# Kernel optimization log

Hardware: AMD Instinct MI355X
Metric: run time of the kernel (lower is better)

## Reference

```python
import jax, jax.numpy as jnp
import numpy as np

N, D, E = 200000, 256, 6400000
RATIO = 0.5
NEG_SLOPE = 0.2


def _xavier(key, shape, gain=1.414):
    fan_in, fan_out = shape[0], shape[1]
    limit = gain * (6.0 / (fan_in + fan_out)) ** 0.5
    return jax.random.uniform(key, shape, jnp.float32, -limit, limit)


def setup_inputs() -> dict:
    key = jax.random.key(0)
    ks = jax.random.split(key, 8)
    x = jax.random.normal(ks[0], (N, D), jnp.float32)
    edge_index = jax.random.randint(ks[1], (2, E), 0, N, dtype=jnp.int64)
    return {
        "x": x,
        "edge_index": edge_index,
        "w_s1": _xavier(ks[2], (2 * D, D)), "b_s1": jnp.zeros((D,), jnp.float32),
        "w_s2": _xavier(ks[3], (D, 1)),     "b_s2": jnp.zeros((1,), jnp.float32),
        "w_f1": _xavier(ks[4], (D, D // 2)), "b_f1": jnp.zeros((D // 2,), jnp.float32),
        "w_f2": _xavier(ks[5], (D // 2, 1)), "b_f2": jnp.zeros((1,), jnp.float32),
        "w_p": _xavier(ks[6], (D, D)),      "b_p": jnp.zeros((D,), jnp.float32),
        "alpha": jnp.float32(0.5), "beta": jnp.float32(0.5),
    }


def reference(x, edge_index, w_s1, b_s1, w_s2, b_s2, w_f1, b_f1, w_f2, b_f2, w_p, b_p, alpha, beta):
    num_nodes = x.shape[0]
    k = max(1, int(RATIO * num_nodes))
    lrelu = lambda v: jax.nn.leaky_relu(v, NEG_SLOPE)

    row, col = edge_index[0], edge_index[1]
    # degree(row, N): scatter-add of ones over source nodes
    deg = jax.ops.segment_sum(jnp.ones_like(row, dtype=x.dtype), row, num_segments=num_nodes)
    # F.normalize(p=2, dim=0) on the [N,1] degree column
    deg_norm = deg / jnp.maximum(jnp.sqrt(jnp.sum(deg * deg)), 1e-12)

    struct_in = jnp.concatenate([x, jnp.broadcast_to(deg_norm[:, None], x.shape)], axis=1)  # [N, 2D]
    struct_scores = (lrelu(struct_in @ w_s1 + b_s1) @ w_s2 + b_s2)[:, 0]  # dropout is eval no-op
    feat_scores = (lrelu(x @ w_f1 + b_f1) @ w_f2 + b_f2)[:, 0]

    a = jax.nn.sigmoid(alpha)
    b = jax.nn.sigmoid(beta)
    s = a + b
    scores = (a / s) * struct_scores + (b / s) * feat_scores  # [N]

    # single-graph top-k (batch=None default path)
    topk_scores, topk_idx = jax.lax.top_k(scores, k)
    x_pooled = lrelu(x[topk_idx] @ w_p + b_p)  # post_pool, dropout no-op

    # edge remap + compaction (valid edges first, -1 padding to keep static shape)
    node_map = jnp.full((num_nodes,), -1, dtype=jnp.int32).at[topk_idx].set(
        jnp.arange(k, dtype=jnp.int32))
    mr, mc = node_map[row], node_map[col]
    mask = (mr >= 0) & (mc >= 0)
    order = jnp.argsort(~mask, stable=True)  # stable: keeps original edge order among valid
    edge_index_pooled = jnp.stack([
        jnp.where(mask, mr, -1)[order],
        jnp.where(mask, mc, -1)[order],
    ])
    return x_pooled, edge_index_pooled, topk_scores
```

## Files before the change

kernel.cpp:

```cpp
#include <hip/hip_runtime.h>
#include <math.h>

typedef unsigned long long u64;
typedef unsigned int u32;
typedef unsigned short u16;
typedef __attribute__((ext_vector_type(8))) short bf16x8;
typedef __attribute__((ext_vector_type(4))) float f32x4;

#define D   256
#define ECH 16
#define EBLK (256*ECH)
#define BAND_W 4096
#define BAND_DELTA 1e-3f
#define HR  25088
#define HCH 32

__device__ __forceinline__ double lrelu(double v){ return v > 0.0 ? v : 0.2*v; }
__device__ __forceinline__ float  lreluf(float v){ return v > 0.0f ? v : 0.2f*v; }

__device__ __forceinline__ u16 f2bf(float f){
  union{float f; u32 u;} v; v.f = f;
  u32 r = v.u + 0x7FFFu + ((v.u >> 16) & 1u);
  return (u16)(r >> 16);
}
__device__ __forceinline__ float bf2f(u16 b){
  union{u32 u; float f;} v; v.u = ((u32)b) << 16; return v.f;
}

__global__ __launch_bounds__(256) void k_deghist(const int* __restrict__ row, int E,
                                                 u32* __restrict__ partial, int NR){
  __shared__ u32 h[HR/2];
  const int tid = threadIdx.x;
  const int r = blockIdx.x % NR;
  const int c = blockIdx.x / NR;
  for (int i = tid; i < HR/2; i += 256) h[i] = 0;
  __syncthreads();
  const int lo = r * HR;
  int CE = ((E + HCH - 1) / HCH + 3) & ~3;
  const int e0 = c * CE;
  const int e1 = min(e0 + CE, E);
  for (int e = e0 + tid*4; e < e1; e += 256*4){
    if (e + 3 < e1){
      int4 v = *(const int4*)(row + e);
      u32 d0 = (u32)(v.x - lo), d1 = (u32)(v.y - lo);
      u32 d2 = (u32)(v.z - lo), d3 = (u32)(v.w - lo);
      if (d0 < (u32)HR) atomicAdd(&h[d0 >> 1], 1u << ((d0 & 1)*16));
      if (d1 < (u32)HR) atomicAdd(&h[d1 >> 1], 1u << ((d1 & 1)*16));
      if (d2 < (u32)HR) atomicAdd(&h[d2 >> 1], 1u << ((d2 & 1)*16));
      if (d3 < (u32)HR) atomicAdd(&h[d3 >> 1], 1u << ((d3 & 1)*16));
    } else {
      for (int j = 0; j < 4 && e + j < e1; ++j){
        u32 d = (u32)(row[e+j] - lo);
        if (d < (u32)HR) atomicAdd(&h[d >> 1], 1u << ((d & 1)*16));
      }
    }
  }
  __syncthreads();
  u32* plane = partial + (size_t)blockIdx.x * (HR/2);
  for (int i = tid; i < HR/2; i += 256) plane[i] = h[i];
}

__global__ void k_degred2(const u32* __restrict__ partial, int N, int NR,
                          int* __restrict__ deg, u64* __restrict__ out){
  __shared__ u64 sh[256];
  u64 local = 0;
  int stride = gridDim.x*blockDim.x;
  for (int i = blockIdx.x*blockDim.x + threadIdx.x; i < N; i += stride){
    int r = i / HR, off = i % HR;
    const int word = off >> 1, shift = (off & 1)*16;
    u32 s = 0;
    #pragma unroll 8
    for (int c = 0; c < HCH; ++c)
      s += (partial[(size_t)(c*NR + r)*(HR/2) + word] >> shift) & 0xFFFFu;
    deg[i] = (int)s;
    local += (u64)s * (u64)s;
  }
  sh[threadIdx.x] = local; __syncthreads();
  for (int s = 128; s > 0; s >>= 1){
    if (threadIdx.x < s) sh[threadIdx.x] += sh[threadIdx.x+s];
    __syncthreads();
  }
  if (threadIdx.x == 0) atomicAdd(out, sh[0]);
}

__global__ void k_prep_wsw(const float* __restrict__ wS1, const float* __restrict__ wF1,
                           const float* __restrict__ wP,
                           const float* __restrict__ alpha, const float* __restrict__ beta,
                           const u64* __restrict__ sumsq,
                           u16* __restrict__ wswH, u16* __restrict__ wswL,
                           u16* __restrict__ wPH,
                           double* __restrict__ s1b, double* __restrict__ scal,
                           float* __restrict__ s1bf, float* __restrict__ scalf){
  const int b = blockIdx.x;
  if (b < 384){
    int idx = b*256 + threadIdx.x;
    int i    = idx & 7;
    int lane = (idx >> 3) & 63;
    int sg   = (idx >> 9) & 7;
    int t    = idx >> 12;
    int k = sg*32 + ((lane >> 4) & 3)*8 + i;
    int c16 = lane & 15;
    float wv;
    if (t < 16) wv = wS1[k*256 + t*16 + c16];
    else        wv = wF1[k*128 + (t-16)*16 + c16];
    u16 h = f2bf(wv);
    wswH[idx] = h;
    wswL[idx] = f2bf(wv - bf2f(h));
  } else if (b < 640){
    int idx = (b-384)*256 + threadIdx.x;
    int i    = idx & 7;
    int lane = (idx >> 3) & 63;
    int sg   = (idx >> 9) & 7;
    int t    = idx >> 12;
    int k = sg*32 + ((lane >> 4) & 3)*8 + i;
    wPH[idx] = f2bf(wP[k*256 + t*16 + (lane & 15)]);
  } else {
    int j = threadIdx.x;
    double s = 0.0;
    for (int r = 0; r < D; ++r) s += (double)wS1[(D + r)*D + j];
    s1b[j] = s;
    s1bf[j] = (float)s;
    if (j == 0){
      double a = 1.0/(1.0 + exp(-(double)alpha[0]));
      double bb = 1.0/(1.0 + exp(-(double)beta[0]));
      scal[0] = a/(a+bb);
      scal[1] = bb/(a+bb);
      double dn = sqrt((double)(*sumsq));
      scal[2] = dn > 1e-12 ? dn : 1e-12;
      scalf[0] = (float)scal[0];
      scalf[1] = (float)scal[1];
      scalf[2] = (float)(1.0/scal[2]);
    }
  }
}

__global__ __launch_bounds__(512, 4) void k_scores_mfma(
    const float* __restrict__ x, const int* __restrict__ deg,
    const u16* __restrict__ wswH, const u16* __restrict__ wswL,
    const float* __restrict__ bS1, const float* __restrict__ wS2, const float* __restrict__ bS2,
    const float* __restrict__ bF1, const float* __restrict__ wF2, const float* __restrict__ bF2,
    const float* __restrict__ s1bf, const float* __restrict__ scalf,
    float* __restrict__ s32, u64* __restrict__ keys, int N, int SORTN)
{
  __shared__ u16 xsh[2][4096];
  __shared__ u16 xsl[2][4096];
  __shared__ float dnsh[64];
  __shared__ float part_s[64][9];
  __shared__ float part_f[64][9];

  const int tid  = threadIdx.x;
  const int lane = tid & 63;
  const int w    = tid >> 6;
  const int node0 = blockIdx.x * 64;

  if (node0 >= N){
    if (tid < 64){
      int i = node0 + tid;
      if (i < SORTN) keys[i] = ~0ULL;
    }
    return;
  }

  if (tid < 64){
    int node = node0 + tid;
    dnsh[tid] = (node < N) ? ((float)deg[node] * scalf[2]) : 0.0f;
  }

  const int row_st = tid >> 3;
  const int seg_st = tid & 7;
  const int unit_w = row_st*8 + (seg_st ^ (row_st & 7));
  const float* srcbase = x + (size_t)(node0 + row_st)*D + seg_st*8;
  const bool rv = (node0 + row_st) < N;

  f32x4 acc[4][3];
  #pragma unroll
  for (int m = 0; m < 4; ++m)
    #pragma unroll
    for (int n = 0; n < 3; ++n) acc[m][n] = (f32x4){0.f,0.f,0.f,0.f};

  float xr[8];
  {
    if (rv){
      float4 a = *(const float4*)(srcbase);
      float4 b = *(const float4*)(srcbase + 4);
      xr[0]=a.x; xr[1]=a.y; xr[2]=a.z; xr[3]=a.w;
      xr[4]=b.x; xr[5]=b.y; xr[6]=b.z; xr[7]=b.w;
    } else {
      #pragma unroll
      for (int i = 0; i < 8; ++i) xr[i] = 0.f;
    }
  }

  #pragma unroll
  for (int c = 0; c < 4; ++c){
    const int pb = c & 1;
    {
      u16 h[8];
      #pragma unroll
      for (int i = 0; i < 8; ++i) h[i] = f2bf(xr[i]);
      uint4 H; H.x = (u32)h[0] | ((u32)h[1]<<16); H.y = (u32)h[2] | ((u32)h[3]<<16);
               H.z = (u32)h[4] | ((u32)h[5]<<16); H.w = (u32)h[6] | ((u32)h[7]<<16);
      u16 l[8];
      #pragma unroll
      for (int i = 0; i < 8; ++i) l[i] = f2bf(xr[i] - bf2f(h[i]));
      uint4 L; L.x = (u32)l[0] | ((u32)l[1]<<16); L.y = (u32)l[2] | ((u32)l[3]<<16);
               L.z = (u32)l[4] | ((u32)l[5]<<16); L.w = (u32)l[6] | ((u32)l[7]<<16);
      *(uint4*)&xsh[pb][unit_w*8] = H;
      *(uint4*)&xsl[pb][unit_w*8] = L;
    }
    __syncthreads();
    if (c < 3){
      const float* sn = srcbase + (c+1)*64;
      if (rv){
        float4 a = *(const float4*)(sn);
        float4 b = *(const float4*)(sn + 4);
        xr[0]=a.x; xr[1]=a.y; xr[2]=a.z; xr[3]=a.w;
        xr[4]=b.x; xr[5]=b.y; xr[6]=b.z; xr[7]=b.w;
      }
    }
    #pragma unroll
    for (int s = 0; s < 2; ++s){
      const int sg = c*2 + s;
      bf16x8 ah[4], al[4];
      #pragma unroll
      for (int mt = 0; mt < 4; ++mt){
        int row = mt*16 + (lane & 15);
        int seg = s*4 + (lane >> 4);
        int un  = row*8 + (seg ^ (row & 7));
        ah[mt] = *(const bf16x8*)&xsh[pb][un*8];
        al[mt] = *(const bf16x8*)&xsl[pb][un*8];
      }
      const int t0 = w*3;
      size_t o0 = ((size_t)(t0*8 + sg)*64 + lane)*8;
      bf16x8 bh = *(const bf16x8*)&wswH[o0];
      bf16x8 bl = *(const bf16x8*)&wswL[o0];
      #pragma unroll
      for (int nt = 0; nt < 3; ++nt){
        bf16x8 nbh = bh, nbl = bl;
        if (nt < 2){
          size_t on = ((size_t)((t0+nt+1)*8 + sg)*64 + lane)*8;
          nbh = *(const bf16x8*)&wswH[on];
          nbl = *(const bf16x8*)&wswL[on];
        }
        #pragma unroll
        for (int mt = 0; mt < 4; ++mt){
          acc[mt][nt] = __builtin_amdgcn_mfma_f32_16x16x32_bf16(ah[mt], bh, acc[mt][nt], 0,0,0);
          acc[mt][nt] = __builtin_amdgcn_mfma_f32_16x16x32_bf16(al[mt], bh, acc[mt][nt], 0,0,0);
          acc[mt][nt] = __builtin_amdgcn_mfma_f32_16x16x32_bf16(ah[mt], bl, acc[mt][nt], 0,0,0);
        }
        bh = nbh; bl = nbl;
      }
    }
    if (c < 3) __syncthreads();
  }

  float dnl[4][4];
  #pragma unroll
  for (int mt = 0; mt < 4; ++mt)
    #pragma unroll
    for (int j = 0; j < 4; ++j)
      dnl[mt][j] = dnsh[mt*16 + (lane>>4)*4 + j];

  float ps[4][4], pf[4][4];
  #pragma unroll
  for (int mt = 0; mt < 4; ++mt)
    #pragma unroll
    for (int j = 0; j < 4; ++j){ ps[mt][j] = 0.f; pf[mt][j] = 0.f; }

  #pragma unroll
  for (int nt = 0; nt < 3; ++nt){
    const int t = w*3 + nt;
    const int c16 = lane & 15;
    const bool isS = (t < 16);
    const int col = isS ? t*16 + c16 : (t-16)*16 + c16;
    const float bias = isS ? bS1[col] : bF1[col];
    const float sbv  = isS ? s1bf[col] : 0.f;
    const float vv   = isS ? wS2[col] : wF2[col];
    #pragma unroll
    for (int mt = 0; mt < 4; ++mt){
      #pragma unroll
      for (int j = 0; j < 4; ++j){
        float v = acc[mt][nt][j] + bias + dnl[mt][j]*sbv;
        v = lreluf(v) * vv;
        v += __shfl_xor(v, 1);
        v += __shfl_xor(v, 2);
        v += __shfl_xor(v, 4);
        v += __shfl_xor(v, 8);
        if (isS) ps[mt][j] += v; else pf[mt][j] += v;
      }
    }
  }
  if ((lane & 15) == 0){
    #pragma unroll
    for (int mt = 0; mt < 4; ++mt)
      #pragma unroll
      for (int j = 0; j < 4; ++j){
        int row = mt*16 + (lane>>4)*4 + j;
        part_s[row][w] = ps[mt][j];
        part_f[row][w] = pf[mt][j];
      }
  }
  __syncthreads();
  if (tid < 64){
    int node = node0 + tid;
    if (node < N){
      float sv = 0.f, fv = 0.f;
      #pragma unroll
      for (int ww = 0; ww < 8; ++ww){ sv += part_s[tid][ww]; fv += part_f[tid][ww]; }
      float sc = scalf[0]*(sv + bS2[0]) + scalf[1]*(fv + bF2[0]);
      s32[node] = sc;
      u32 bits = __float_as_uint(sc);
      u32 ord = (bits >> 31) ? ~bits : (bits | 0x80000000u);
      keys[node] = ((u64)(~ord) << 32) | (u32)node;
    } else {
      int i = node0 + tid;
      if (i < SORTN) keys[i] = ~0ULL;
    }
  }
}

__global__ __launch_bounds__(1024) void k_bsort_local8k(u64* __restrict__ keys){
  __shared__ u64 sk[8192];
  const int tid = threadIdx.x;
  const int base = blockIdx.x * 8192;
  #pragma unroll
  for (int e = 0; e < 8; ++e) sk[tid + e*1024] = keys[base + tid + e*1024];
  __syncthreads();
  for (int size = 2; size <= 8192; size <<= 1){
    for (int stride = size >> 1; stride > 0; stride >>= 1){
      #pragma unroll
      for (int pp = 0; pp < 4; ++pp){
        int p  = tid + pp*1024;
        int i  = 2*p - (p & (stride-1));
        int jj = i + stride;
        bool up = (((base + i) & size) == 0);
        u64 ki = sk[i], kj = sk[jj];
        if ((ki > kj) == up){ sk[i] = kj; sk[jj] = ki; }
      }
      __syncthreads();
    }
  }
  #pragma unroll
  for (int e = 0; e < 8; ++e) keys[base + tid + e*1024] = sk[tid + e*1024];
}

__global__ __launch_bounds__(1024) void k_bmerge_local8k(u64* __restrict__ keys, int size){
  __shared__ u64 sk[8192];
  const int tid = threadIdx.x;
  const int base = blockIdx.x * 8192;
  #pragma unroll
  for (int e = 0; e < 8; ++e) sk[tid + e*1024] = keys[base + tid + e*1024];
  __syncthreads();
  for (int stride = 4096; stride > 0; stride >>= 1){
    #pragma unroll
    for (int pp = 0; pp < 4; ++pp){
      int p  = tid + pp*1024;
      int i  = 2*p - (p & (stride-1));
      int jj = i + stride;
      bool up = (((base + i) & size) == 0);
      u64 ki = sk[i], kj = sk[jj];
      if ((ki > kj) == up){ sk[i] = kj; sk[jj] = ki; }
    }
    __syncthreads();
  }
  #pragma unroll
  for (int e = 0; e < 8; ++e) keys[base + tid + e*1024] = sk[tid + e*1024];
}

template<int NS>
__global__ void k_bpassM(u64* __restrict__ keys, int size, int stride){
  const int G = 1 << NS;
  u32 t = blockIdx.x*blockDim.x + threadIdx.x;
  u32 smin = (u32)stride >> (NS-1);
  u32 i0 = (t/smin)*(smin << NS) + (t % smin);
  u64 v[G];
  #pragma unroll
  for (int j = 0; j < G; ++j) v[j] = keys[i0 + (u32)j*smin];
  bool up = ((i0 & (u32)size) == 0);
  #pragma unroll
  for (int b = (G>>1); b >= 1; b >>= 1){
    #pragma unroll
    for (int j = 0; j < G; ++j){
      if ((j & b) == 0){
        u64 a = v[j], cc = v[j|b];
        if ((a > cc) == up){ v[j] = cc; v[j|b] = a; }
      }
    }
  }
  #pragma unroll
  for (int j = 0; j < G; ++j) keys[i0 + (u32)j*smin] = v[j];
}

__global__ void kr_cut(const u64* __restrict__ keys, int k, float* __restrict__ cutbuf,
                       int* __restrict__ r01){
  if (threadIdx.x == 0 && blockIdx.x == 0){
    u32 key32 = (u32)(keys[k-1] >> 32);
    u32 ord = ~key32;
    u32 u = (ord & 0x80000000u) ? (ord ^ 0x80000000u) : ~ord;
    float c = __uint_as_float(u);
    cutbuf[0] = c - BAND_DELTA;
    cutbuf[1] = c + BAND_DELTA;
    r01[0] = 0x7FFFFFFF;
    r01[1] = -1;
  }
}

__global__ __launch_bounds__(256) void kr_rescore(
    const u64* __restrict__ keys, const float* __restrict__ s32,
    const float* __restrict__ x, const int* __restrict__ deg,
    const float* __restrict__ wS1, const float* __restrict__ bS1,
    const float* __restrict__ wS2, const float* __restrict__ bS2,
    const float* __restrict__ wF1, const float* __restrict__ bF1,
    const float* __restrict__ wF2, const float* __restrict__ bF2,
    const double* __restrict__ s1b, const double* __restrict__ scal,
    const float* __restrict__ cutbuf, int* __restrict__ r01,
    double* __restrict__ bandS, int k, int N)
{
  const int r = k - BAND_W + blockIdx.x;
  if (r < 0 || r >= N) return;
  const int node = (int)(u32)(keys[r] & 0xFFFFFFFFULL);
  const float s = s32[node];
  if (s < cutbuf[0] || s > cutbuf[1]) return;

  const int tid = threadIdx.x;
  if (tid == 0){ atomicMin(&r01[0], r); atomicMax(&r01[1], r); }

  __shared__ float xr[256];
  __shared__ double rsp[4], rfp[4];
  xr[tid] = x[(size_t)node*D + tid];
  __syncthreads();

  const int j = tid;
  double a0=0.0, a1=0.0, a2=0.0, a3=0.0;
  double b0=0.0, b1=0.0, b2=0.0, b3=0.0;
  if (j < 128){
    for (int rr = 0; rr < D; rr += 4){
      double x0 = (double)xr[rr+0], x1 = (double)xr[rr+1];
      double x2 = (double)xr[rr+2], x3 = (double)xr[rr+3];
      a0 = fma(x0, (double)wS1[(rr+0)*D + j], a0);
      a1 = fma(x1, (double)wS1[(rr+1)*D + j], a1);
      a2 = fma(x2, (double)wS1[(rr+2)*D + j], a2);
      a3 = fma(x3, (double)wS1[(rr+3)*D + j], a3);
      b0 = fma(x0, (double)wF1[(rr+0)*128 + j], b0);
      b1 = fma(x1, (double)wF1[(rr+1)*128 + j], b1);
      b2 = fma(x2, (double)wF1[(rr+2)*128 + j], b2);
      b3 = fma(x3, (double)wF1[(rr+3)*128 + j], b3);
    }
  } else {
    for (int rr = 0; rr < D; rr += 4){
      double x0 = (double)xr[rr+0], x1 = (double)xr[rr+1];
      double x2 = (double)xr[rr+2], x3 = (double)xr[rr+3];
      a0 = fma(x0, (double)wS1[(rr+0)*D + j], a0);
      a1 = fma(x1, (double)wS1[(rr+1)*D + j], a1);
      a2 = fma(x2, (double)wS1[(rr+2)*D + j], a2);
      a3 = fma(x3, (double)wS1[(rr+3)*D + j], a3);
    }
  }
  double accA = ((a0+a1)+(a2+a3)) + (double)bS1[j] + ((double)deg[node]/scal[2]) * s1b[j];
  double sp = lrelu(accA) * (double)wS2[j];
  double fp = 0.0;
  if (j < 128){
    double accB = ((b0+b1)+(b2+b3)) + (double)bF1[j];
    fp = lrelu(accB) * (double)wF2[j];
  }

  const int lane = tid & 63, wave = tid >> 6;
  #pragma unroll
  for (int off = 32; off > 0; off >>= 1){
    sp += __shfl_down(sp, off);
    fp += __shfl_down(fp, off);
  }
  if (lane == 0){ rsp[wave] = sp; rfp[wave] = fp; }
  __syncthreads();
  if (tid == 0){
    double SP = rsp[0]+rsp[1]+rsp[2]+rsp[3];
    double FP = rfp[0]+rfp[1]+rfp[2]+rfp[3];
    bandS[blockIdx.x] = scal[0]*(SP + (double)bS2[0]) + scal[1]*(FP + (double)bF2[0]);
  }
}

__global__ __launch_bounds__(1024) void kr_bandsort(u64* __restrict__ keys,
    const double* __restrict__ bandS, const int* __restrict__ r01, int k){
  __shared__ double bs[8192];
  __shared__ int bi[8192];
  const int r0 = r01[0], r1 = r01[1];
  int nb = r1 - r0 + 1;
  if (nb <= 1) return;
  if (nb > 8192) nb = 8192;
  int M = 1; while (M < nb) M <<= 1;
  const int tid = threadIdx.x;
  const int sbase = r0 - (k - BAND_W);
  for (int m = tid; m < M; m += 1024){
    if (m < nb){ bs[m] = bandS[sbase + m]; bi[m] = (int)(u32)(keys[r0+m] & 0xFFFFFFFFULL); }
    else       { bs[m] = -1.0/0.0;         bi[m] = 0x7FFFFFFF; }
  }
  __syncthreads();
  for (int size = 2; size <= M; size <<= 1){
    for (int stride = size >> 1; stride > 0; stride >>= 1){
      for (int p = tid; p < (M >> 1); p += 1024){
        int i = 2*p - (p & (stride-1));
        int jj = i + stride;
        bool up = ((i & size) == 0);
        double si_ = bs[i], sj = bs[jj];
        int ii = bi[i], ij = bi[jj];
        bool gt = (si_ < sj) || (si_ == sj && ii > ij);
        if (gt == up){ bs[i]=sj; bs[jj]=si_; bi[i]=ij; bi[jj]=ii; }
      }
      __syncthreads();
    }
  }
  for (int m = tid; m < nb; m += 1024)
    keys[r0+m] = (u64)(u32)bi[m];
}

__global__ void k_finalize(const u64* __restrict__ keys, const float* __restrict__ s32,
                           int k, int* __restrict__ nmap, float* __restrict__ outS){
  int p = blockIdx.x*blockDim.x + threadIdx.x;
  if (p < k){
    int node = (int)(u32)(keys[p] & 0xFFFFFFFFULL);
    nmap[node] = p;
    outS[p] = s32[node];
  }
}

__global__ __launch_bounds__(512, 4) void k_xpool_mfma(
    const float* __restrict__ x, const u64* __restrict__ keys,
    const u16* __restrict__ wH,
    const float* __restrict__ bP, float* __restrict__ out, int kk)
{
  __shared__ u16 xsh[2][4096];

  const int tid  = threadIdx.x;
  const int lane = tid & 63;
  const int w    = tid >> 6;
  const int p0 = blockIdx.x * 64;
  if (p0 >= kk) return;

  const int row_st = tid >> 3;
  const int seg_st = tid & 7;
  const int unit_w = row_st*8 + (seg_st ^ (row_st & 7));
  int prow = p0 + row_st; if (prow >= kk) prow = kk - 1;
  const int node = (int)(u32)(keys[prow] & 0xFFFFFFFFULL);
  const float* srcbase = x + (size_t)node*D + seg_st*8;

  f32x4 acc[4][2];
  #pragma unroll
  for (int m = 0; m < 4; ++m){ acc[m][0] = (f32x4){0.f,0.f,0.f,0.f}; acc[m][1] = (f32x4){0.f,0.f,0.f,0.f}; }

  float xr[8];
  {
    float4 a = *(const float4*)(srcbase);
    float4 b = *(const float4*)(srcbase + 4);
    xr[0]=a.x; xr[1]=a.y; xr[2]=a.z; xr[3]=a.w;
    xr[4]=b.x; xr[5]=b.y; xr[6]=b.z; xr[7]=b.w;
  }

  #pragma unroll
  for (int c = 0; c < 4; ++c){
    const int pb = c & 1;
    {
      u16 h[8];
      #pragma unroll
      for (int i = 0; i < 8; ++i) h[i] = f2bf(xr[i]);
      uint4 H; H.x = (u32)h[0] | ((u32)h[1]<<16); H.y = (u32)h[2] | ((u32)h[3]<<16);
               H.z = (u32)h[4] | ((u32)h[5]<<16); H.w = (u32)h[6] | ((u32)h[7]<<16);
      *(uint4*)&xsh[pb][unit_w*8] = H;
    }
    __syncthreads();
    if (c < 3){
      const float* sn = srcbase + (c+1)*64;
      float4 a = *(const float4*)(sn);
      float4 b = *(const float4*)(sn + 4);
      xr[0]=a.x; xr[1]=a.y; xr[2]=a.z; xr[3]=a.w;
      xr[4]=b.x; xr[5]=b.y; xr[6]=b.z; xr[7]=b.w;
    }
    #pragma unroll
    for (int s = 0; s < 2; ++s){
      const int sg = c*2 + s;
      bf16x8 ah[4];
      #pragma unroll
      for (int mt = 0; mt < 4; ++mt){
        int row = mt*16 + (lane & 15);
        int seg = s*4 + (lane >> 4);
        int un  = row*8 + (seg ^ (row & 7));
        ah[mt] = *(const bf16x8*)&xsh[pb][un*8];
      }
      const int t0 = w*2;
      size_t o0 = ((size_t)(t0*8 + sg)*64 + lane)*8;
      bf16x8 bh = *(const bf16x8*)&wH[o0];
      #pragma unroll
      for (int nt = 0; nt < 2; ++nt){
        bf16x8 nbh = bh;
        if (nt < 1){
          size_t on = ((size_t)((t0+1)*8 + sg)*64 + lane)*8;
          nbh = *(const bf16x8*)&wH[on];
        }
        #pragma unroll
        for (int mt = 0; mt < 4; ++mt)
          acc[mt][nt] = __builtin_amdgcn_mfma_f32_16x16x32_bf16(ah[mt], bh, acc[mt][nt], 0,0,0);
        bh = nbh;
      }
    }
    if (c < 3) __syncthreads();
  }

  const int c16 = lane & 15, r4 = (lane >> 4)*4;
  #pragma unroll
  for (int nt = 0; nt < 2; ++nt){
    const int col = (w*2 + nt)*16 + c16;
    const float bias = bP[col];
    #pragma unroll
    for (int mt = 0; mt < 4; ++mt){
      #pragma unroll
      for (int j = 0; j < 4; ++j){
        int p = p0 + mt*16 + r4 + j;
        if (p < kk) out[(size_t)p*D + col] = lreluf(acc[mt][nt][j] + bias);
      }
    }
  }
}

__global__ __launch_bounds__(256) void k_ecount(const int* __restrict__ erow, const int* __restrict__ ecol,
    const int* __restrict__ nmap, int E, int* __restrict__ bcount){
  __shared__ int sc[256];
  const int tid = threadIdx.x;
  const int base = blockIdx.x*EBLK + tid*ECH;
  int cnt = 0;
  #pragma unroll
  for (int q = 0; q < ECH; ++q){
    int e = base + q;
    if (e < E){
      if (nmap[erow[e]] >= 0 && nmap[ecol[e]] >= 0) cnt++;
    }
  }
  sc[tid] = cnt; __syncthreads();
  for (int s = 128; s > 0; s >>= 1){
    if (tid < s) sc[tid] += sc[tid+s];
    __syncthreads();
  }
  if (tid == 0) bcount[blockIdx.x] = sc[0];
}

__global__ __launch_bounds__(1024) void k_escan(const int* __restrict__ bcount, int nblk,
                                                int* __restrict__ boff, int* __restrict__ tot){
  __shared__ int sh[1024];
  const int tid = threadIdx.x;
  int carry = 0;
  for (int s = 0; s < nblk; s += 1024){
    int v = (s + tid < nblk) ? bcount[s+tid] : 0;
    sh[tid] = v; __syncthreads();
    for (int d = 1; d < 1024; d <<= 1){
      int t = (tid >= d) ? sh[tid-d] : 0;
      __syncthreads();
      sh[tid] += t;
      __syncthreads();
    }
    if (s + tid < nblk) boff[s+tid] = carry + sh[tid] - v;
    carry += sh[1023];
    __syncthreads();
  }
  if (tid == 0) *tot = carry;
}

__global__ void k_efill_tail(float* __restrict__ outR, float* __restrict__ outC,
                             const int* __restrict__ tot, int E){
  const int t0 = *tot;
  int stride = gridDim.x*blockDim.x;
  for (int i = t0 + blockIdx.x*blockDim.x + threadIdx.x; i < E; i += stride){
    outR[i] = -1.0f;
    outC[i] = -1.0f;
  }
}

__global__ __launch_bounds__(256) void k_escatter(const int* __restrict__ erow, const int* __restrict__ ecol,
    const int* __restrict__ nmap, int E, const int* __restrict__ boff,
    float* __restrict__ outR, float* __restrict__ outC){
  __shared__ int sc[256];
  const int tid = threadIdx.x;
  const int base = blockIdx.x*EBLK + tid*ECH;
  int mr[ECH], mc[ECH];
  int cnt = 0;
  #pragma unroll
  for (int q = 0; q < ECH; ++q){
    int e = base + q;
    int a = -1, b = -1;
    if (e < E){ a = nmap[erow[e]]; b = nmap[ecol[e]]; }
    mr[q] = a; mc[q] = b;
    if (a >= 0 && b >= 0) cnt++;
  }
  sc[tid] = cnt; __syncthreads();
  int v = cnt;
  for (int d = 1; d < 256; d <<= 1){
    int t = (tid >= d) ? sc[tid-d] : 0;
    __syncthreads();
    sc[tid] += t;
    __syncthreads();
  }
  int pos = boff[blockIdx.x] + sc[tid] - v;
  #pragma unroll
  for (int q = 0; q < ECH; ++q){
    if (mr[q] >= 0 && mc[q] >= 0){
      outR[pos] = (float)mr[q];
      outC[pos] = (float)mc[q];
      pos++;
    }
  }
}

extern "C" void kernel_launch(void* const* d_in, const int* in_sizes, int n_in,
                              void* d_out, int out_size, void* d_ws, size_t ws_size,
                              hipStream_t stream)
{
  const float* x   = (const float*)d_in[0];
  const int*   ei  = (const int*)d_in[1];
  const float* wS1 = (const float*)d_in[2];
  const float* bS1 = (const float*)d_in[3];
  const float* wS2 = (const float*)d_in[4];
  const float* bS2 = (const float*)d_in[5];
  const float* wF1 = (const float*)d_in[6];
  const float* bF1 = (const float*)d_in[7];
  const float* wF2 = (const float*)d_in[8];
  const float* bF2 = (const float*)d_in[9];
  const float* wP  = (const float*)d_in[10];
  const float* bP  = (const float*)d_in[11];
  const float* alpha = (const float*)d_in[12];
  const float* beta  = (const float*)d_in[13];
  (void)n_in; (void)out_size; (void)ws_size;

  const int N = in_sizes[0] / D;
  const int E = in_sizes[1] / 2;
  int k = (int)(0.5 * (double)N); if (k < 1) k = 1;
  int SORTN = 8192; while (SORTN < N) SORTN <<= 1;
  const int nblk_e = (E + EBLK - 1) / EBLK;
  const int NR = (N + HR - 1) / HR;

  char* w = (char*)d_ws;
  size_t off = 0;
  auto alloc = [&](size_t bytes)->char*{
    char* p = w + off;
    off = (off + bytes + 255) & ~(size_t)255;
    return p;
  };
  float*  s32    = (float*) alloc((size_t)N*4);
  u64*    keys   = (u64*)   alloc((size_t)SORTN*8);
  int*    deg    = (int*)   alloc((size_t)N*4);
  int*    nmap   = (int*)   alloc((size_t)N*4);
  double* s1b    = (double*)alloc((size_t)D*8);
  float*  s1bf   = (float*) alloc((size_t)D*4);
  double* scal   = (double*)alloc(4*8);
  float*  scalf  = (float*) alloc(4*4);
  u64*    sumsq  = (u64*)   alloc(8);
  float*  cutbuf = (float*) alloc(2*4);
  int*    r01    = (int*)   alloc(2*4);
  int*    tot    = (int*)   alloc(4);
  double* bandS  = (double*)alloc((size_t)2*BAND_W*8);
  u16*    wswH   = (u16*)   alloc((size_t)98304*2);
  u16*    wswL   = (u16*)   alloc((size_t)98304*2);
  u16*    wswPH  = (u16*)   alloc((size_t)65536*2);
  int*    bcount = (int*)   alloc((size_t)nblk_e*4);
  int*    boff   = (int*)   alloc((size_t)nblk_e*4);

  float* outX  = (float*)d_out;
  float* outER = outX  + (size_t)k*D;
  float* outEC = outER + (size_t)E;
  float* outS  = outEC + (size_t)E;

  u32* partial = (u32*)outER;

  hipMemsetAsync(sumsq, 0,    8,           stream);
  hipMemsetAsync(nmap,  0xFF, (size_t)N*4, stream);

  k_deghist<<<NR*HCH, 256, 0, stream>>>(ei, E, partial, NR);
  k_degred2<<<1024, 256, 0, stream>>>(partial, N, NR, deg, sumsq);
  k_prep_wsw<<<641, 256, 0, stream>>>(wS1, wF1, wP, alpha, beta, sumsq,
                                      wswH, wswL, wswPH,
                                      s1b, scal, s1bf, scalf);
  k_scores_mfma<<<SORTN/64, 512, 0, stream>>>(x, deg, wswH, wswL,
                                              bS1, wS2, bS2, bF1, wF2, bF2,
                                              s1bf, scalf, s32, keys, N, SORTN);

  k_bsort_local8k<<<SORTN/8192, 1024, 0, stream>>>(keys);
  for (int size = 16384; size <= SORTN; size <<= 1){
    int stride = size >> 1;
    while (stride >= 8192){
      int ns = 1;
      while (ns < 4 && (stride >> ns) >= 8192) ns++;
      switch (ns){
        case 1: k_bpassM<1><<<SORTN/2/256,  256, 0, stream>>>(keys, size, stride); break;
        case 2: k_bpassM<2><<<SORTN/4/256,  256, 0, stream>>>(keys, size, stride); break;
        case 3: k_bpassM<3><<<SORTN/8/256,  256, 0, stream>>>(keys, size, stride); break;
        default:k_bpassM<4><<<SORTN/16/256, 256, 0, stream>>>(keys, size, stride); break;
      }
      stride >>= ns;
    }
    k_bmerge_local8k<<<SORTN/8192, 1024, 0, stream>>>(keys, size);
  }

  kr_cut     <<<1, 64, 0, stream>>>(keys, k, cutbuf, r01);
  kr_rescore <<<2*BAND_W, 256, 0, stream>>>(keys, s32, x, deg, wS1,bS1,wS2,bS2,
                                            wF1,bF1,wF2,bF2, s1b, scal,
                                            cutbuf, r01, bandS, k, N);
  kr_bandsort<<<1, 1024, 0, stream>>>(keys, bandS, r01, k);

  k_finalize<<<(k+255)/256, 256, 0, stream>>>(keys, s32, k, nmap, outS);
  k_xpool_mfma<<<(k+63)/64, 512, 0, stream>>>(x, keys, wswPH, bP, outX, k);
  k_ecount  <<<nblk_e, 256, 0, stream>>>(ei, ei+E, nmap, E, bcount);
  k_escan   <<<1, 1024, 0, stream>>>(bcount, nblk_e, boff, tot);
  k_efill_tail<<<1024, 256, 0, stream>>>(outER, outEC, tot, E);
  k_escatter<<<nblk_e, 256, 0, stream>>>(ei, ei+E, nmap, E, boff, outER, outEC);
}
```

Baseline: 751.3 us.

## Replace bitonic sort with 64K-bucket histogram scatter and pack degree histogram into bytes

```diff
diff --git a/kernel.cpp b/kernel.cpp
--- a/kernel.cpp
+++ b/kernel.cpp
@@ -10,10 +10,11 @@
 #define D   256
 #define ECH 16
 #define EBLK (256*ECH)
-#define BAND_W 4096
+#define BAND_W 2048
 #define BAND_DELTA 1e-3f
-#define HR  25088
-#define HCH 32
+#define HR  50176
+#define HCH 64
+#define NBUCK 65536
 
 __device__ __forceinline__ double lrelu(double v){ return v > 0.0 ? v : 0.2*v; }
 __device__ __forceinline__ float  lreluf(float v){ return v > 0.0f ? v : 0.2f*v; }
@@ -29,11 +30,11 @@
 
 __global__ __launch_bounds__(256) void k_deghist(const int* __restrict__ row, int E,
                                                  u32* __restrict__ partial, int NR){
-  __shared__ u32 h[HR/2];
+  __shared__ u32 h[HR/4];
   const int tid = threadIdx.x;
   const int r = blockIdx.x % NR;
   const int c = blockIdx.x / NR;
-  for (int i = tid; i < HR/2; i += 256) h[i] = 0;
+  for (int i = tid; i < HR/4; i += 256) h[i] = 0;
   __syncthreads();
   const int lo = r * HR;
   int CE = ((E + HCH - 1) / HCH + 3) & ~3;
@@ -44,20 +45,20 @@
       int4 v = *(const int4*)(row + e);
       u32 d0 = (u32)(v.x - lo), d1 = (u32)(v.y - lo);
       u32 d2 = (u32)(v.z - lo), d3 = (u32)(v.w - lo);
-      if (d0 < (u32)HR) atomicAdd(&h[d0 >> 1], 1u << ((d0 & 1)*16));
-      if (d1 < (u32)HR) atomicAdd(&h[d1 >> 1], 1u << ((d1 & 1)*16));
-      if (d2 < (u32)HR) atomicAdd(&h[d2 >> 1], 1u << ((d2 & 1)*16));
-      if (d3 < (u32)HR) atomicAdd(&h[d3 >> 1], 1u << ((d3 & 1)*16));
+      if (d0 < (u32)HR) atomicAdd(&h[d0 >> 2], 1u << ((d0 & 3)*8));
+      if (d1 < (u32)HR) atomicAdd(&h[d1 >> 2], 1u << ((d1 & 3)*8));
+      if (d2 < (u32)HR) atomicAdd(&h[d2 >> 2], 1u << ((d2 & 3)*8));
+      if (d3 < (u32)HR) atomicAdd(&h[d3 >> 2], 1u << ((d3 & 3)*8));
     } else {
       for (int j = 0; j < 4 && e + j < e1; ++j){
         u32 d = (u32)(row[e+j] - lo);
-        if (d < (u32)HR) atomicAdd(&h[d >> 1], 1u << ((d & 1)*16));
+        if (d < (u32)HR) atomicAdd(&h[d >> 2], 1u << ((d & 3)*8));
       }
     }
   }
   __syncthreads();
-  u32* plane = partial + (size_t)blockIdx.x * (HR/2);
-  for (int i = tid; i < HR/2; i += 256) plane[i] = h[i];
+  u32* plane = partial + (size_t)blockIdx.x * (HR/4);
+  for (int i = tid; i < HR/4; i += 256) plane[i] = h[i];
 }
 
 __global__ void k_degred2(const u32* __restrict__ partial, int N, int NR,
@@ -67,11 +68,11 @@
   int stride = gridDim.x*blockDim.x;
   for (int i = blockIdx.x*blockDim.x + threadIdx.x; i < N; i += stride){
     int r = i / HR, off = i % HR;
-    const int word = off >> 1, shift = (off & 1)*16;
+    const int word = off >> 2, shift = (off & 3)*8;
     u32 s = 0;
     #pragma unroll 8
     for (int c = 0; c < HCH; ++c)
-      s += (partial[(size_t)(c*NR + r)*(HR/2) + word] >> shift) & 0xFFFFu;
+      s += (partial[(size_t)(c*NR + r)*(HR/4) + word] >> shift) & 0xFFu;
     deg[i] = (int)s;
     local += (u64)s * (u64)s;
   }
@@ -140,7 +141,7 @@
     const float* __restrict__ bS1, const float* __restrict__ wS2, const float* __restrict__ bS2,
     const float* __restrict__ bF1, const float* __restrict__ wF2, const float* __restrict__ bF2,
     const float* __restrict__ s1bf, const float* __restrict__ scalf,
-    float* __restrict__ s32, u64* __restrict__ keys, int N, int SORTN)
+    float* __restrict__ s32, u64* __restrict__ keysrc, u32* __restrict__ kmm, int N)
 {
   __shared__ u16 xsh[2][4096];
   __shared__ u16 xsl[2][4096];
@@ -152,14 +153,6 @@
   const int lane = tid & 63;
   const int w    = tid >> 6;
   const int node0 = blockIdx.x * 64;
-
-  if (node0 >= N){
-    if (tid < 64){
-      int i = node0 + tid;
-      if (i < SORTN) keys[i] = ~0ULL;
-    }
-    return;
-  }
 
   if (tid < 64){
     int node = node0 + tid;
@@ -303,6 +296,7 @@
   __syncthreads();
   if (tid < 64){
     int node = node0 + tid;
+    u32 key32mn = 0xFFFFFFFFu, key32mx = 0u;
     if (node < N){
       float sv = 0.f, fv = 0.f;
       #pragma unroll
@@ -311,84 +305,75 @@
       s32[node] = sc;
       u32 bits = __float_as_uint(sc);
       u32 ord = (bits >> 31) ? ~bits : (bits | 0x80000000u);
-      keys[node] = ((u64)(~ord) << 32) | (u32)node;
-    } else {
-      int i = node0 + tid;
-      if (i < SORTN) keys[i] = ~0ULL;
-    }
-  }
-}
-
-__global__ __launch_bounds__(1024) void k_bsort_local8k(u64* __restrict__ keys){
-  __shared__ u64 sk[8192];
-  const int tid = threadIdx.x;
-  const int base = blockIdx.x * 8192;
-  #pragma unroll
-  for (int e = 0; e < 8; ++e) sk[tid + e*1024] = keys[base + tid + e*1024];
-  __syncthreads();
-  for (int size = 2; size <= 8192; size <<= 1){
-    for (int stride = size >> 1; stride > 0; stride >>= 1){
-      #pragma unroll
-      for (int pp = 0; pp < 4; ++pp){
-        int p  = tid + pp*1024;
-        int i  = 2*p - (p & (stride-1));
-        int jj = i + stride;
-        bool up = (((base + i) & size) == 0);
-        u64 ki = sk[i], kj = sk[jj];
-        if ((ki > kj) == up){ sk[i] = kj; sk[jj] = ki; }
-      }
-      __syncthreads();
-    }
-  }
-  #pragma unroll
-  for (int e = 0; e < 8; ++e) keys[base + tid + e*1024] = sk[tid + e*1024];
-}
-
-__global__ __launch_bounds__(1024) void k_bmerge_local8k(u64* __restrict__ keys, int size){
-  __shared__ u64 sk[8192];
-  const int tid = threadIdx.x;
-  const int base = blockIdx.x * 8192;
-  #pragma unroll
-  for (int e = 0; e < 8; ++e) sk[tid + e*1024] = keys[base + tid + e*1024];
-  __syncthreads();
-  for (int stride = 4096; stride > 0; stride >>= 1){
-    #pragma unroll
-    for (int pp = 0; pp < 4; ++pp){
-      int p  = tid + pp*1024;
-      int i  = 2*p - (p & (stride-1));
-      int jj = i + stride;
-      bool up = (((base + i) & size) == 0);
-      u64 ki = sk[i], kj = sk[jj];
-      if ((ki > kj) == up){ sk[i] = kj; sk[jj] = ki; }
-    }
-    __syncthreads();
-  }
-  #pragma unroll
-  for (int e = 0; e < 8; ++e) keys[base + tid + e*1024] = sk[tid + e*1024];
-}
-
-template<int NS>
-__global__ void k_bpassM(u64* __restrict__ keys, int size, int stride){
-  const int G = 1 << NS;
-  u32 t = blockIdx.x*blockDim.x + threadIdx.x;
-  u32 smin = (u32)stride >> (NS-1);
-  u32 i0 = (t/smin)*(smin << NS) + (t % smin);
-  u64 v[G];
-  #pragma unroll
-  for (int j = 0; j < G; ++j) v[j] = keys[i0 + (u32)j*smin];
-  bool up = ((i0 & (u32)size) == 0);
-  #pragma unroll
-  for (int b = (G>>1); b >= 1; b >>= 1){
-    #pragma unroll
-    for (int j = 0; j < G; ++j){
-      if ((j & b) == 0){
-        u64 a = v[j], cc = v[j|b];
-        if ((a > cc) == up){ v[j] = cc; v[j|b] = a; }
-      }
-    }
-  }
-  #pragma unroll
-  for (int j = 0; j < G; ++j) keys[i0 + (u32)j*smin] = v[j];
+      u32 key32 = ~ord;
+      keysrc[node] = ((u64)key32 << 32) | (u32)node;
+      key32mn = key32; key32mx = key32;
+    }
+    #pragma unroll
+    for (int off = 32; off > 0; off >>= 1){
+      u32 on = __shfl_xor(key32mn, off);
+      u32 ox = __shfl_xor(key32mx, off);
+      key32mn = min(key32mn, on);
+      key32mx = max(key32mx, ox);
+    }
+    if (tid == 0){
+      atomicMin(&kmm[0], key32mn);
+      atomicMax(&kmm[1], key32mx);
+    }
+  }
+}
+
+__global__ void k_hist(const u64* __restrict__ keysrc, int N,
+                       const u32* __restrict__ kmm, u32* __restrict__ hist){
+  const u32 kmin = kmm[0];
+  const u64 rng = (u64)(kmm[1] - kmm[0]) + 1;
+  int stride = gridDim.x*blockDim.x;
+  for (int i = blockIdx.x*blockDim.x + threadIdx.x; i < N; i += stride){
+    u32 key = (u32)(keysrc[i] >> 32);
+    u32 b = (u32)((((u64)(key - kmin)) << 16) / rng);
+    atomicAdd(&hist[b], 1u);
+  }
+}
+
+__global__ __launch_bounds__(1024) void k_scan64k(const u32* __restrict__ hist,
+                                                  u32* __restrict__ boff){
+  __shared__ u32 ts[1024];
+  const int t = threadIdx.x;
+  u32 loc[64];
+  u32 s = 0;
+  const uint4* hp = (const uint4*)(hist + t*64);
+  #pragma unroll
+  for (int i = 0; i < 16; ++i){
+    uint4 v = hp[i];
+    loc[i*4+0]=v.x; loc[i*4+1]=v.y; loc[i*4+2]=v.z; loc[i*4+3]=v.w;
+    s += v.x + v.y + v.z + v.w;
+  }
+  ts[t] = s; __syncthreads();
+  for (int d = 1; d < 1024; d <<= 1){
+    u32 v = (t >= d) ? ts[t-d] : 0;
+    __syncthreads();
+    ts[t] += v;
+    __syncthreads();
+  }
+  u32 run = ts[t] - s;
+  u32* bp = boff + t*64;
+  #pragma unroll 8
+  for (int i = 0; i < 64; ++i){ bp[i] = run; run += loc[i]; }
+}
+
+__global__ void k_scatter(const u64* __restrict__ keysrc, int N,
+                          const u32* __restrict__ kmm, u32* __restrict__ boff,
+                          u64* __restrict__ keyS){
+  const u32 kmin = kmm[0];
+  const u64 rng = (u64)(kmm[1] - kmm[0]) + 1;
+  int stride = gridDim.x*blockDim.x;
+  for (int i = blockIdx.x*blockDim.x + threadIdx.x; i < N; i += stride){
+    u64 kv = keysrc[i];
+    u32 key = (u32)(kv >> 32);
+    u32 b = (u32)((((u64)(key - kmin)) << 16) / rng);
+    u32 pos = atomicAdd(&boff[b], 1u);
+    keyS[pos] = kv;
+  }
 }
 
 __global__ void kr_cut(const u64* __restrict__ keys, int k, float* __restrict__ cutbuf,
@@ -420,7 +405,10 @@
   if (r < 0 || r >= N) return;
   const int node = (int)(u32)(keys[r] & 0xFFFFFFFFULL);
   const float s = s32[node];
-  if (s < cutbuf[0] || s > cutbuf[1]) return;
+  if (s < cutbuf[0] || s > cutbuf[1]){
+    if (threadIdx.x == 0) bandS[blockIdx.x] = (double)s;
+    return;
+  }
 
   const int tid = threadIdx.x;
   if (tid == 0){ atomicMin(&r01[0], r); atomicMax(&r01[1], r); }
@@ -481,12 +469,12 @@
 
 __global__ __launch_bounds__(1024) void kr_bandsort(u64* __restrict__ keys,
     const double* __restrict__ bandS, const int* __restrict__ r01, int k){
-  __shared__ double bs[8192];
-  __shared__ int bi[8192];
+  __shared__ double bs[4096];
+  __shared__ int bi[4096];
   const int r0 = r01[0], r1 = r01[1];
   int nb = r1 - r0 + 1;
   if (nb <= 1) return;
-  if (nb > 8192) nb = 8192;
+  if (nb > 4096) nb = 4096;
   int M = 1; while (M < nb) M <<= 1;
   const int tid = threadIdx.x;
   const int sbase = r0 - (k - BAND_W);
@@ -730,7 +718,6 @@
   const int N = in_sizes[0] / D;
   const int E = in_sizes[1] / 2;
   int k = (int)(0.5 * (double)N); if (k < 1) k = 1;
-  int SORTN = 8192; while (SORTN < N) SORTN <<= 1;
   const int nblk_e = (E + EBLK - 1) / EBLK;
   const int NR = (N + HR - 1) / HR;
 
@@ -742,9 +729,13 @@
     return p;
   };
   float*  s32    = (float*) alloc((size_t)N*4);
-  u64*    keys   = (u64*)   alloc((size_t)SORTN*8);
+  u64*    keysrc = (u64*)   alloc((size_t)N*8);
+  u64*    keyS   = (u64*)   alloc((size_t)N*8);
   int*    deg    = (int*)   alloc((size_t)N*4);
   int*    nmap   = (int*)   alloc((size_t)N*4);
+  u32*    kmm    = (u32*)   alloc(2*4);
+  u32*    hist   = (u32*)   alloc((size_t)NBUCK*4);
+  u32*    boffH  = (u32*)   alloc((size_t)NBUCK*4);
   double* s1b    = (double*)alloc((size_t)D*8);
   float*  s1bf   = (float*) alloc((size_t)D*4);
   double* scal   = (double*)alloc(4*8);
@@ -767,43 +758,33 @@
 
   u32* partial = (u32*)outER;
 
-  hipMemsetAsync(sumsq, 0,    8,           stream);
-  hipMemsetAsync(nmap,  0xFF, (size_t)N*4, stream);
+  hipMemsetAsync(sumsq, 0,    8,               stream);
+  hipMemsetAsync(nmap,  0xFF, (size_t)N*4,     stream);
+  hipMemsetAsync(kmm,   0xFF, 4,               stream);
+  hipMemsetAsync(kmm+1, 0x00, 4,               stream);
+  hipMemsetAsync(hist,  0,    (size_t)NBUCK*4, stream);
 
   k_deghist<<<NR*HCH, 256, 0, stream>>>(ei, E, partial, NR);
   k_degred2<<<1024, 256, 0, stream>>>(partial, N, NR, deg, sumsq);
   k_prep_wsw<<<641, 256, 0, stream>>>(wS1, wF1, wP, alpha, beta, sumsq,
                                       wswH, wswL, wswPH,
                                       s1b, scal, s1bf, scalf);
-  k_scores_mfma<<<SORTN/64, 512, 0, stream>>>(x, deg, wswH, wswL,
-                                              bS1, wS2, bS2, bF1, wF2, bF2,
-                                              s1bf, scalf, s32, keys, N, SORTN);
-
-  k_bsort_local8k<<<SORTN/8192, 1024, 0, stream>>>(keys);
-  for (int size = 16384; size <= SORTN; size <<= 1){
-    int stride = size >> 1;
-    while (stride >= 8192){
-      int ns = 1;
-      while (ns < 4 && (stride >> ns) >= 8192) ns++;
-      switch (ns){
-        case 1: k_bpassM<1><<<SORTN/2/256,  256, 0, stream>>>(keys, size, stride); break;
-        case 2: k_bpassM<2><<<SORTN/4/256,  256, 0, stream>>>(keys, size, stride); break;
-        case 3: k_bpassM<3><<<SORTN/8/256,  256, 0, stream>>>(keys, size, stride); break;
-        default:k_bpassM<4><<<SORTN/16/256, 256, 0, stream>>>(keys, size, stride); break;
-      }
-      stride >>= ns;
-    }
-    k_bmerge_local8k<<<SORTN/8192, 1024, 0, stream>>>(keys, size);
-  }
-
-  kr_cut     <<<1, 64, 0, stream>>>(keys, k, cutbuf, r01);
-  kr_rescore <<<2*BAND_W, 256, 0, stream>>>(keys, s32, x, deg, wS1,bS1,wS2,bS2,
+  k_scores_mfma<<<(N + 63)/64, 512, 0, stream>>>(x, deg, wswH, wswL,
+                                                 bS1, wS2, bS2, bF1, wF2, bF2,
+                                                 s1bf, scalf, s32, keysrc, kmm, N);
+
+  k_hist   <<<(N+255)/256, 256, 0, stream>>>(keysrc, N, kmm, hist);
+  k_scan64k<<<1, 1024, 0, stream>>>(hist, boffH);
+  k_scatter<<<(N+255)/256, 256, 0, stream>>>(keysrc, N, kmm, boffH, keyS);
+
+  kr_cut     <<<1, 64, 0, stream>>>(keyS, k, cutbuf, r01);
+  kr_rescore <<<2*BAND_W, 256, 0, stream>>>(keyS, s32, x, deg, wS1,bS1,wS2,bS2,
                                             wF1,bF1,wF2,bF2, s1b, scal,
                                             cutbuf, r01, bandS, k, N);
-  kr_bandsort<<<1, 1024, 0, stream>>>(keys, bandS, r01, k);
-
-  k_finalize<<<(k+255)/256, 256, 0, stream>>>(keys, s32, k, nmap, outS);
-  k_xpool_mfma<<<(k+63)/64, 512, 0, stream>>>(x, keys, wswPH, bP, outX, k);
+  kr_bandsort<<<1, 1024, 0, stream>>>(keyS, bandS, r01, k);
+
+  k_finalize<<<(k+255)/256, 256, 0, stream>>>(keyS, s32, k, nmap, outS);
+  k_xpool_mfma<<<(k+63)/64, 512, 0, stream>>>(x, keyS, wswPH, bP, outX, k);
   k_ecount  <<<nblk_e, 256, 0, stream>>>(ei, ei+E, nmap, E, bcount);
   k_escan   <<<1, 1024, 0, stream>>>(bcount, nblk_e, boff, tot);
   k_efill_tail<<<1024, 256, 0, stream>>>(outER, outEC, tot, E);
```

Result: faster. 690.0 us (-8.2%).
